# Kernel tuning notes

Measured on AMD Instinct MI355X. Metric: run time of the kernel, lower is better.

## Reference

```python
import jax, jax.numpy as jnp
import numpy as np

BETA = 0.25


def setup_inputs() -> dict:
    key = jax.random.key(0)
    k1, k2 = jax.random.split(key)
    x = jax.random.normal(k1, (8, 256, 2048), dtype=jnp.float32)        # (B, C, L)
    codebook = jax.random.normal(k2, (8192, 256), dtype=jnp.float32)    # (K, C)
    return {"x": x, "codebook": codebook}


def reference(x, codebook):
    # x: (B, C, L) -> xt: (B, L, C)
    xt = jnp.transpose(x, (0, 2, 1))
    # Euclidean distances via ||a||^2 + ||b||^2 - 2 a.b (matches torch.cdist p=2)
    x_sq = jnp.sum(xt * xt, axis=-1, keepdims=True)          # (B, L, 1)
    c_sq = jnp.sum(codebook * codebook, axis=-1)             # (K,)
    dots = jnp.einsum('blc,kc->blk', xt, codebook)           # (B, L, K)
    dists = jnp.sqrt(jnp.maximum(x_sq + c_sq[None, None, :] - 2.0 * dots, 0.0))
    # NOTE: original code uses argmax over distances (faithfully reproduced)
    code = jnp.argmax(dists, axis=2)                         # (B, L) int
    emb = jnp.transpose(codebook[code], (0, 2, 1))           # (B, C, L)
    sg = jax.lax.stop_gradient
    loss = jnp.mean((sg(x) - emb) ** 2 + BETA * (sg(emb) - emb) ** 2)
    return code, emb, loss
```

## Files before the change

kernel.cpp:

```cpp
#include <hip/hip_runtime.h>
#include <hip/hip_fp16.h>
#include <stdint.h>

typedef unsigned int u32;
typedef unsigned long long u64;
typedef unsigned short ushort_t;

#define B_ 8
#define C_ 256
#define L_ 2048
#define K_ 8192
#define M_ 16384

#define WS_KEYS   0
#define WS_CNT    131072
#define WS_MAXCS  131076
#define WS_LOSS   131080
#define WS_XSQ    131328
#define WS_CSQ    196864
#define WS_LIST   295168
#define WS_LMAX   4489472
#define WS_XTH    12878080
#define WS_CBH    21266688
#define LIST_CAP  1048576u

typedef __attribute__((ext_vector_type(8))) short s8v;
typedef __attribute__((ext_vector_type(4))) float f4v;

__device__ __forceinline__ ushort_t f2bf(float f) {
  u32 u = __float_as_uint(f);
  u32 r = (u + 0x7FFFu + ((u >> 16) & 1u)) >> 16;
  return (ushort_t)r;
}

__device__ __forceinline__ void gld16(void* lds, const void* g) {
  __builtin_amdgcn_global_load_lds(
      (const __attribute__((address_space(1))) u32*)g,
      (__attribute__((address_space(3))) u32*)lds, 16, 0, 0);
}


__global__ void __launch_bounds__(256)
vq_transpose(const float* __restrict__ x, float* __restrict__ xtf,
             ushort_t* __restrict__ xth) {
  __shared__ float t[64][65];
  int tid = threadIdx.x;
  int b  = blockIdx.x >> 7;
  int cc = (blockIdx.x >> 5) & 3;
  int lc = blockIdx.x & 31;
#pragma unroll
  for (int j = 0; j < 4; ++j) {
    int c  = (tid >> 4) + j * 16;
    int lq = tid & 15;
    float4 v = *(const float4*)&x[((size_t)(b * C_ + cc * 64 + c)) * L_ + lc * 64 + lq * 4];
    t[c][lq * 4 + 0] = v.x; t[c][lq * 4 + 1] = v.y;
    t[c][lq * 4 + 2] = v.z; t[c][lq * 4 + 3] = v.w;
  }
  __syncthreads();
  int l = tid >> 2, qc = tid & 3;
  size_t m = (size_t)b * L_ + lc * 64 + l;
#pragma unroll
  for (int j = 0; j < 4; ++j) {
    int q = qc + j * 4;
    float4 v = make_float4(t[q * 4 + 0][l], t[q * 4 + 1][l],
                           t[q * 4 + 2][l], t[q * 4 + 3][l]);
    *(float4*)&xtf[m * C_ + cc * 64 + q * 4] = v;
    ushort4 h;
    h.x = f2bf(v.x); h.y = f2bf(v.y); h.z = f2bf(v.z); h.w = f2bf(v.w);
    *(ushort4*)&xth[m * C_ + cc * 64 + q * 4] = h;
  }
}

__global__ void vq_xsqt(const float* __restrict__ xtf, float* __restrict__ xsq) {
  int t = threadIdx.x;
  int m = blockIdx.x * 16 + (t >> 4);
  int g = t & 15;
  const float* row = xtf + (size_t)m * C_;
  float s = 0.0f;
#pragma unroll
  for (int j = 0; j < 4; ++j) {
    float4 v = *(const float4*)&row[g * 4 + j * 64];
    s += v.x * v.x + v.y * v.y + v.z * v.z + v.w * v.w;
  }
#pragma unroll
  for (int off = 1; off < 16; off <<= 1) s += __shfl_xor(s, off, 64);
  if (g == 0) xsq[m] = s;
}

__global__ void vq_cbprep(const float* __restrict__ cb, float* __restrict__ csq,
                          int* __restrict__ maxcs, ushort_t* __restrict__ cbh) {
  int t = threadIdx.x;
  int k = blockIdx.x * 16 + (t >> 4);
  int g = t & 15;
  const float* row = cb + (size_t)k * C_;
  float s = 0.0f;
#pragma unroll
  for (int j = 0; j < 4; ++j) {
    float4 v = *(const float4*)&row[g * 4 + j * 64];
    s += v.x * v.x + v.y * v.y + v.z * v.z + v.w * v.w;
    ushort4 h;
    h.x = f2bf(v.x); h.y = f2bf(v.y); h.z = f2bf(v.z); h.w = f2bf(v.w);
    *(ushort4*)&cbh[(size_t)k * C_ + g * 4 + j * 64] = h;
  }
#pragma unroll
  for (int off = 1; off < 16; off <<= 1) s += __shfl_xor(s, off, 64);
  if (g == 0) {
    csq[k] = s;
    atomicMax(maxcs, __float_as_int(s));
  }
}


#define STAGE(buf, s_)                                                        \
  {                                                                           \
    const int t_ = (s_) >> 1, kh_ = (s_) & 1;                                 \
    _Pragma("unroll")                                                         \
    for (int q = 0; q < 4; ++q) {                                             \
      int chunk = (q * 8 + w) * 64 + l;             \
      int row = chunk >> 4;                                       \
      int csrc = lr ^ (row & 7);                                              \
      gld16(&Bs[(buf)][chunk * 8],                                            \
            &cbh[(size_t)(n0 + t_ * 128 + row) * 256 + kh_ * 128 + csrc * 8]);\
    }                                                                         \
  }

__global__ void __launch_bounds__(512, 2)
vq_gemm(const ushort_t* __restrict__ xth, const ushort_t* __restrict__ cbh,
        const float* __restrict__ csq, __half* __restrict__ lmax) {
  __shared__ short Bs[2][128 * 128];

  const int tid = threadIdx.x;
  const int w = tid >> 6, l = tid & 63;
  const int lr = l & 15, lk = l >> 4;
  const int strip = blockIdx.x >> 3, ns = blockIdx.x & 7;
  const int r0 = strip * 256 + w * 32;
  const int n0 = ns * 1024;

  s8v a[2][8];
#pragma unroll
  for (int i = 0; i < 2; ++i)
#pragma unroll
    for (int ks = 0; ks < 8; ++ks)
      a[i][ks] = *(const s8v*)&xth[(size_t)(r0 + i * 16 + lr) * 256 + ks * 32 + lk * 8];

  f4v acc[2][8];
  STAGE(0, 0);
  __syncthreads();

  for (int s = 0; s < 16; ++s) {
    const int buf = s & 1;
    const int kh = s & 1, tt = s >> 1;
    if (s < 15) STAGE(buf ^ 1, s + 1);

    if (kh == 0) {
#pragma unroll
      for (int i = 0; i < 2; ++i)
#pragma unroll
        for (int j = 0; j < 8; ++j) acc[i][j] = (f4v){0.f, 0.f, 0.f, 0.f};
    }

#pragma unroll
    for (int ks = 0; ks < 4; ++ks) {
      s8v b[8];
#pragma unroll
      for (int j = 0; j < 8; ++j)
        b[j] = *(const s8v*)&Bs[buf][(j * 16 + lr) * 128 + (((ks * 4 + lk) ^ (lr & 7)) * 8)];
#pragma unroll
      for (int i = 0; i < 2; ++i)
#pragma unroll
        for (int j = 0; j < 8; ++j)
          acc[i][j] = __builtin_amdgcn_mfma_f32_16x16x32_bf16(b[j], a[i][kh * 4 + ks], acc[i][j], 0, 0, 0);
    }

    if (kh == 1) {
      float vm[2][4];
#pragma unroll
      for (int jp = 0; jp < 4; ++jp) {
        float4 cqa = *(const float4*)&csq[n0 + tt * 128 + jp * 32 + lk * 4];
        float4 cqb = *(const float4*)&csq[n0 + tt * 128 + jp * 32 + 16 + lk * 4];
#pragma unroll
        for (int i = 0; i < 2; ++i) {
          f4v A0 = acc[i][2 * jp], A1 = acc[i][2 * jp + 1];
          float m0 = fmaxf(fmaxf(__fmaf_rn(-2.0f, A0[0], cqa.x),
                                 __fmaf_rn(-2.0f, A0[1], cqa.y)),
                           fmaxf(__fmaf_rn(-2.0f, A0[2], cqa.z),
                                 __fmaf_rn(-2.0f, A0[3], cqa.w)));
          float m1 = fmaxf(fmaxf(__fmaf_rn(-2.0f, A1[0], cqb.x),
                                 __fmaf_rn(-2.0f, A1[1], cqb.y)),
                           fmaxf(__fmaf_rn(-2.0f, A1[2], cqb.z),
                                 __fmaf_rn(-2.0f, A1[3], cqb.w)));
          float vmx = fmaxf(m0, m1);
          vmx = fmaxf(vmx, __shfl_xor(vmx, 16, 64));
          vmx = fmaxf(vmx, __shfl_xor(vmx, 32, 64));
          vm[i][jp] = vmx;
        }
      }
      if (l < 16) {
#pragma unroll
        for (int i = 0; i < 2; ++i) {
          short4 sv;
          sv.x = (short)__half_as_ushort(__float2half(vm[i][0]));
          sv.y = (short)__half_as_ushort(__float2half(vm[i][1]));
          sv.z = (short)__half_as_ushort(__float2half(vm[i][2]));
          sv.w = (short)__half_as_ushort(__float2half(vm[i][3]));
          *(short4*)&lmax[(size_t)(r0 + i * 16 + l) * 256 + ns * 32 + tt * 4] = sv;
        }
      }
    }
    __syncthreads();
  }
}

__global__ void __launch_bounds__(256)
vq_thr(const __half* __restrict__ lmax, const float* __restrict__ xsq,
       const int* __restrict__ maxcs, u32* __restrict__ list, u32* __restrict__ cnt) {
  __shared__ u32 wcnt[4];
  __shared__ u32 gbase_s;
  const int t = threadIdx.x, w = t >> 6, l = t & 63;
  const int m0 = blockIdx.x * 64 + w * 16;
  const float mc = __int_as_float(*maxcs);

  ushort4 hv[16];
  float thv[16];
  u32 wtot = 0;
#pragma unroll
  for (int i = 0; i < 16; ++i) {
    int m = m0 + i;
    hv[i] = *(const ushort4*)&lmax[(size_t)m * 256 + l * 4];
    float v0 = __half2float(__ushort_as_half(hv[i].x));
    float v1 = __half2float(__ushort_as_half(hv[i].y));
    float v2 = __half2float(__ushort_as_half(hv[i].z));
    float v3 = __half2float(__ushort_as_half(hv[i].w));
    float g = fmaxf(fmaxf(v0, v1), fmaxf(v2, v3));
#pragma unroll
    for (int off = 1; off < 64; off <<= 1) g = fmaxf(g, __shfl_xor(g, off, 64));
    float th = g - (0.033f * sqrtf(xsq[m] * mc) + 0.6f);
    thv[i] = th;
    wtot += __popcll(__ballot(v0 >= th));
    wtot += __popcll(__ballot(v1 >= th));
    wtot += __popcll(__ballot(v2 >= th));
    wtot += __popcll(__ballot(v3 >= th));
  }
  if (l == 0) wcnt[w] = wtot;
  __syncthreads();
  if (t == 0) gbase_s = atomicAdd(cnt, wcnt[0] + wcnt[1] + wcnt[2] + wcnt[3]);
  __syncthreads();
  u32 off = gbase_s;
  for (int ww = 0; ww < w; ++ww) off += wcnt[ww];
#pragma unroll
  for (int i = 0; i < 16; ++i) {
    int m = m0 + i;
    float th = thv[i];
    float v[4];
    v[0] = __half2float(__ushort_as_half(hv[i].x));
    v[1] = __half2float(__ushort_as_half(hv[i].y));
    v[2] = __half2float(__ushort_as_half(hv[i].z));
    v[3] = __half2float(__ushort_as_half(hv[i].w));
#pragma unroll
    for (int j = 0; j < 4; ++j) {
      u64 mask = __ballot(v[j] >= th);
      if (v[j] >= th) {
        u32 pos = off + (u32)__popcll(mask & ((1ull << l) - 1ull));
        if (pos < LIST_CAP) list[pos] = ((u32)m << 8) | (u32)(l * 4 + j);
      }
      off += (u32)__popcll(mask);
    }
  }
}

__global__ void __launch_bounds__(256)
vq_rescore(const u32* __restrict__ list, const u32* __restrict__ cnt,
           const float* __restrict__ xtf, const float* __restrict__ cb,
           const float* __restrict__ xsq, const float* __restrict__ csq,
           u64* __restrict__ keys) {
  u32 n = *cnt; if (n > LIST_CAP) n = LIST_CAP;
  const int l = threadIdx.x & 63;
  const int u = l & 7;
  const int g = l >> 3;
  int wid = (blockIdx.x * 256 + threadIdx.x) >> 6;
  int nw = (gridDim.x * 256) >> 6;
  for (u32 e = wid; e < n; e += nw) {
    u32 ent = list[e];
    int m = (int)(ent >> 8), blk = (int)(ent & 255u);
    float4 xv[8];
#pragma unroll
    for (int i = 0; i < 8; ++i)
      xv[i] = *(const float4*)&xtf[(size_t)m * C_ + (i * 8 + u) * 4];
    float xq = xsq[m];
    u64 bestkey = 0;
#pragma unroll
    for (int cc = 0; cc < 4; ++cc) {
      int k = blk * 32 + cc * 8 + g;
      const float* crow = &cb[(size_t)k * C_];
      float p = 0.0f;
#pragma unroll
      for (int i = 0; i < 8; ++i) {
        float4 cv = *(const float4*)&crow[(i * 8 + u) * 4];
        p += xv[i].x * cv.x + xv[i].y * cv.y + xv[i].z * cv.z + xv[i].w * cv.w;
      }
#pragma unroll
      for (int off = 1; off < 8; off <<= 1) p += __shfl_xor(p, off, 64);
      if (u == 0) {
        float d2 = __fsub_rn(__fadd_rn(xq, csq[k]), __fmul_rn(2.0f, p));
        float dist = sqrtf(fmaxf(d2, 0.0f));
        u64 key = ((u64)__float_as_uint(dist) << 32) |
                  (u64)(0xFFFFFFFFu - (u32)k);
        if (key > bestkey) bestkey = key;
      }
    }
#pragma unroll
    for (int off = 8; off < 64; off <<= 1) {
      u64 o = __shfl_xor(bestkey, off, 64);
      if (o > bestkey) bestkey = o;
    }
    if (l == 0) atomicMax(&keys[m], bestkey);
  }
}


__global__ void __launch_bounds__(256)
vq_gather(const u64* __restrict__ keys, const float* __restrict__ cb,
          const float* __restrict__ x, float* __restrict__ out_code,
          float* __restrict__ emb, float* __restrict__ loss_acc) {
  __shared__ float rows[32 * 260];
  __shared__ int codes_s[32];
  __shared__ float partial[4];
  int t = threadIdx.x;
  int b = blockIdx.x >> 6;
  int l0 = (blockIdx.x & 63) * 32;
  if (t < 32) {
    u64 key = keys[b * L_ + l0 + t];
    int code = (int)(0xFFFFFFFFu - (u32)(key & 0xFFFFFFFFull));
    codes_s[t] = code;
    out_code[b * L_ + l0 + t] = (float)code;
  }
  __syncthreads();
  {
    int r = t >> 3, c4 = t & 7;
    const float* src = cb + (size_t)codes_s[r] * C_;
#pragma unroll
    for (int j = 0; j < 8; ++j) {
      float4 v = *(const float4*)&src[(c4 + 8 * j) * 4];
      *(float4*)&rows[r * 260 + (c4 + 8 * j) * 4] = v;
    }
  }
  __syncthreads();
  float ls = 0.0f;
  int l = t & 31, cg = t >> 5;
#pragma unroll 4
  for (int cs = 0; cs < 32; ++cs) {
    int c = cg * 32 + cs;
    float v = rows[l * 260 + c];
    size_t gi = (size_t)(b * C_ + c) * L_ + l0 + l;
    emb[gi] = v;
    float d = x[gi] - v;
    ls = fmaf(d, d, ls);
  }
#pragma unroll
  for (int off = 1; off < 64; off <<= 1) ls += __shfl_xor(ls, off, 64);
  if ((t & 63) == 0) partial[t >> 6] = ls;
  __syncthreads();
  if (t == 0)
    atomicAdd(loss_acc, partial[0] + partial[1] + partial[2] + partial[3]);
}

__global__ void vq_loss(const float* __restrict__ loss_acc, float* __restrict__ out) {
  out[0] = loss_acc[0] / 4194304.0f;
}

extern "C" void kernel_launch(void* const* d_in, const int* in_sizes, int n_in,
                              void* d_out, int out_size, void* d_ws, size_t ws_size,
                              hipStream_t stream) {
  const float* x  = (const float*)d_in[0];
  const float* cb = (const float*)d_in[1];
  float* out = (float*)d_out;
  char* ws = (char*)d_ws;

  u64* keys      = (u64*)(ws + WS_KEYS);
  u32* cnt       = (u32*)(ws + WS_CNT);
  int* maxcs     = (int*)(ws + WS_MAXCS);
  float* loss_a  = (float*)(ws + WS_LOSS);
  float* xsq     = (float*)(ws + WS_XSQ);
  float* csq     = (float*)(ws + WS_CSQ);
  u32* list      = (u32*)(ws + WS_LIST);
  __half* lmax   = (__half*)(ws + WS_LMAX);
  ushort_t* xth  = (ushort_t*)(ws + WS_XTH);
  ushort_t* cbh  = (ushort_t*)(ws + WS_CBH);
  float* xtf     = out + M_;

  hipMemsetAsync(ws, 0, 131084, stream);

  vq_transpose<<<1024, 256, 0, stream>>>(x, xtf, xth);
  vq_cbprep<<<K_ / 16, 256, 0, stream>>>(cb, csq, maxcs, cbh);
  vq_xsqt<<<M_ / 16, 256, 0, stream>>>(xtf, xsq);
  vq_gemm<<<512, 512, 0, stream>>>(xth, cbh, csq, lmax);
  vq_thr<<<256, 256, 0, stream>>>(lmax, xsq, maxcs, list, cnt);
  vq_rescore<<<2048, 256, 0, stream>>>(list, cnt, xtf, cb, xsq, csq, keys);
  vq_gather<<<(B_ * L_) / 32, 256, 0, stream>>>(keys, cb, x, out, out + M_, loss_a);
  vq_loss<<<1, 1, 0, stream>>>(loss_a, out + M_ + (size_t)B_ * C_ * L_);
}
```

Before: 251.5 us.

## Retile VQ distance GEMM to 64x64 warp tiles with full-depth codebook staging

Each warp now computes a 64-row by 64-code tile instead of 32 rows by 128 codes, with warps arranged 4x2. Each stage loads 128 codebook rows at the full channel depth of 256 rather than splitting channels into two halves. The grid shrinks to 256 blocks, each covering 2048 codes. This halves the LDS B-fragment reads per MFMA and removes half the stages and barriers. In exchange it doubles the x-fragment registers and LDS to 128KB per block, which likely limits each CU to one block.

```diff
diff --git a/kernel.cpp b/kernel.cpp
--- a/kernel.cpp
+++ b/kernel.cpp
@@ -111,100 +111,96 @@
 }
 
 
-#define STAGE(buf, s_)                                                        \
+#define STAGE(buf, t_)                                                        \
   {                                                                           \
-    const int t_ = (s_) >> 1, kh_ = (s_) & 1;                                 \
     _Pragma("unroll")                                                         \
-    for (int q = 0; q < 4; ++q) {                                             \
-      int chunk = (q * 8 + w) * 64 + l;             \
-      int row = chunk >> 4;                                       \
-      int csrc = lr ^ (row & 7);                                              \
-      gld16(&Bs[(buf)][chunk * 8],                                            \
-            &cbh[(size_t)(n0 + t_ * 128 + row) * 256 + kh_ * 128 + csrc * 8]);\
+    for (int q = 0; q < 8; ++q) {                                             \
+      int codeT = (w * 8 + q) * 2 + (l >> 5);                                 \
+      int chunk = l & 31;                                                     \
+      gld16(&Bs[(buf)][(w * 8 + q) * 512],                                    \
+            &cbh[(size_t)(n0 + (t_) * 128 + codeT) * 256 +                    \
+                 ((chunk ^ (codeT & 7)) * 8)]);                               \
     }                                                                         \
   }
 
 __global__ void __launch_bounds__(512, 2)
 vq_gemm(const ushort_t* __restrict__ xth, const ushort_t* __restrict__ cbh,
         const float* __restrict__ csq, __half* __restrict__ lmax) {
-  __shared__ short Bs[2][128 * 128];
+  __shared__ short Bs[2][128 * 256];
 
   const int tid = threadIdx.x;
   const int w = tid >> 6, l = tid & 63;
   const int lr = l & 15, lk = l >> 4;
-  const int strip = blockIdx.x >> 3, ns = blockIdx.x & 7;
-  const int r0 = strip * 256 + w * 32;
-  const int n0 = ns * 1024;
-
-  s8v a[2][8];
-#pragma unroll
-  for (int i = 0; i < 2; ++i)
+  const int wr = w >> 1, wc = w & 1;
+  const int strip = blockIdx.x >> 2, ns = blockIdx.x & 3;
+  const int r0 = strip * 256 + wr * 64;
+  const int n0 = ns * 2048;
+
+  s8v a[4][8];
+#pragma unroll
+  for (int i = 0; i < 4; ++i)
 #pragma unroll
     for (int ks = 0; ks < 8; ++ks)
       a[i][ks] = *(const s8v*)&xth[(size_t)(r0 + i * 16 + lr) * 256 + ks * 32 + lk * 8];
 
-  f4v acc[2][8];
   STAGE(0, 0);
   __syncthreads();
 
-  for (int s = 0; s < 16; ++s) {
-    const int buf = s & 1;
-    const int kh = s & 1, tt = s >> 1;
-    if (s < 15) STAGE(buf ^ 1, s + 1);
-
-    if (kh == 0) {
-#pragma unroll
-      for (int i = 0; i < 2; ++i)
-#pragma unroll
-        for (int j = 0; j < 8; ++j) acc[i][j] = (f4v){0.f, 0.f, 0.f, 0.f};
-    }
-
-#pragma unroll
-    for (int ks = 0; ks < 4; ++ks) {
-      s8v b[8];
-#pragma unroll
-      for (int j = 0; j < 8; ++j)
-        b[j] = *(const s8v*)&Bs[buf][(j * 16 + lr) * 128 + (((ks * 4 + lk) ^ (lr & 7)) * 8)];
-#pragma unroll
-      for (int i = 0; i < 2; ++i)
-#pragma unroll
-        for (int j = 0; j < 8; ++j)
-          acc[i][j] = __builtin_amdgcn_mfma_f32_16x16x32_bf16(b[j], a[i][kh * 4 + ks], acc[i][j], 0, 0, 0);
-    }
-
-    if (kh == 1) {
-      float vm[2][4];
-#pragma unroll
-      for (int jp = 0; jp < 4; ++jp) {
-        float4 cqa = *(const float4*)&csq[n0 + tt * 128 + jp * 32 + lk * 4];
-        float4 cqb = *(const float4*)&csq[n0 + tt * 128 + jp * 32 + 16 + lk * 4];
-#pragma unroll
-        for (int i = 0; i < 2; ++i) {
-          f4v A0 = acc[i][2 * jp], A1 = acc[i][2 * jp + 1];
-          float m0 = fmaxf(fmaxf(__fmaf_rn(-2.0f, A0[0], cqa.x),
-                                 __fmaf_rn(-2.0f, A0[1], cqa.y)),
-                           fmaxf(__fmaf_rn(-2.0f, A0[2], cqa.z),
-                                 __fmaf_rn(-2.0f, A0[3], cqa.w)));
-          float m1 = fmaxf(fmaxf(__fmaf_rn(-2.0f, A1[0], cqb.x),
-                                 __fmaf_rn(-2.0f, A1[1], cqb.y)),
-                           fmaxf(__fmaf_rn(-2.0f, A1[2], cqb.z),
-                                 __fmaf_rn(-2.0f, A1[3], cqb.w)));
-          float vmx = fmaxf(m0, m1);
-          vmx = fmaxf(vmx, __shfl_xor(vmx, 16, 64));
-          vmx = fmaxf(vmx, __shfl_xor(vmx, 32, 64));
-          vm[i][jp] = vmx;
-        }
-      }
-      if (l < 16) {
-#pragma unroll
-        for (int i = 0; i < 2; ++i) {
-          short4 sv;
-          sv.x = (short)__half_as_ushort(__float2half(vm[i][0]));
-          sv.y = (short)__half_as_ushort(__float2half(vm[i][1]));
-          sv.z = (short)__half_as_ushort(__float2half(vm[i][2]));
-          sv.w = (short)__half_as_ushort(__float2half(vm[i][3]));
-          *(short4*)&lmax[(size_t)(r0 + i * 16 + l) * 256 + ns * 32 + tt * 4] = sv;
-        }
+  for (int t = 0; t < 16; ++t) {
+    const int buf = t & 1;
+    if (t < 15) STAGE(buf ^ 1, t + 1);
+
+    f4v acc[4][4];
+#pragma unroll
+    for (int i = 0; i < 4; ++i)
+#pragma unroll
+      for (int j = 0; j < 4; ++j) acc[i][j] = (f4v){0.f, 0.f, 0.f, 0.f};
+
+#pragma unroll
+    for (int ks = 0; ks < 8; ++ks) {
+      s8v b[4];
+#pragma unroll
+      for (int j = 0; j < 4; ++j) {
+        int row = wc * 64 + j * 16 + lr;
+        b[j] = *(const s8v*)&Bs[buf][row * 256 + (((ks * 4 + lk) ^ (lr & 7)) * 8)];
+      }
+#pragma unroll
+      for (int i = 0; i < 4; ++i)
+#pragma unroll
+        for (int j = 0; j < 4; ++j)
+          acc[i][j] = __builtin_amdgcn_mfma_f32_16x16x32_bf16(b[j], a[i][ks], acc[i][j], 0, 0, 0);
+    }
+
+    const int cbase = n0 + t * 128 + wc * 64;
+    float vm[4][2];
+#pragma unroll
+    for (int jp = 0; jp < 2; ++jp) {
+      float4 cqa = *(const float4*)&csq[cbase + jp * 32 + lk * 4];
+      float4 cqb = *(const float4*)&csq[cbase + jp * 32 + 16 + lk * 4];
+#pragma unroll
+      for (int i = 0; i < 4; ++i) {
+        f4v A0 = acc[i][2 * jp], A1 = acc[i][2 * jp + 1];
+        float m0 = fmaxf(fmaxf(__fmaf_rn(-2.0f, A0[0], cqa.x),
+                               __fmaf_rn(-2.0f, A0[1], cqa.y)),
+                         fmaxf(__fmaf_rn(-2.0f, A0[2], cqa.z),
+                               __fmaf_rn(-2.0f, A0[3], cqa.w)));
+        float m1 = fmaxf(fmaxf(__fmaf_rn(-2.0f, A1[0], cqb.x),
+                               __fmaf_rn(-2.0f, A1[1], cqb.y)),
+                         fmaxf(__fmaf_rn(-2.0f, A1[2], cqb.z),
+                               __fmaf_rn(-2.0f, A1[3], cqb.w)));
+        float vmx = fmaxf(m0, m1);
+        vmx = fmaxf(vmx, __shfl_xor(vmx, 16, 64));
+        vmx = fmaxf(vmx, __shfl_xor(vmx, 32, 64));
+        vm[i][jp] = vmx;
+      }
+    }
+    if (l < 16) {
+#pragma unroll
+      for (int i = 0; i < 4; ++i) {
+        short2 sv;
+        sv.x = (short)__half_as_ushort(__float2half(vm[i][0]));
+        sv.y = (short)__half_as_ushort(__float2half(vm[i][1]));
+        *(short2*)&lmax[(size_t)(r0 + i * 16 + l) * 256 + ns * 64 + t * 4 + wc * 2] = sv;
       }
     }
     __syncthreads();
@@ -393,7 +389,7 @@
   vq_transpose<<<1024, 256, 0, stream>>>(x, xtf, xth);
   vq_cbprep<<<K_ / 16, 256, 0, stream>>>(cb, csq, maxcs, cbh);
   vq_xsqt<<<M_ / 16, 256, 0, stream>>>(xtf, xsq);
-  vq_gemm<<<512, 512, 0, stream>>>(xth, cbh, csq, lmax);
+  vq_gemm<<<256, 512, 0, stream>>>(xth, cbh, csq, lmax);
   vq_thr<<<256, 256, 0, stream>>>(lmax, xsq, maxcs, list, cnt);
   vq_rescore<<<2048, 256, 0, stream>>>(list, cnt, xtf, cb, xsq, csq, keys);
   vq_gather<<<(B_ * L_) / 32, 256, 0, stream>>>(keys, cb, x, out, out + M_, loss_a);
```

Measured after the change: 248.3 us. No clear change (-1.2%).
